# Performance work log

Measured on AMD Instinct MI355X. Metric: run time of the kernel, lower is better.

Reference implementation:

```python
import jax, jax.numpy as jnp
import numpy as np

DYADIC_LEVELS = 3
SIG_LEVEL = 3  # hardcoded depth-3 truncated signature (matches init_kwargs)


def path_signature(inc):
    """Truncated (level-3) path signature of a piecewise-linear path.

    inc: [..., N, d] increments. Returns [..., d + d^2 + d^3] flattened
    signature (levels 1..3, row-major tensor flattening, no scalar term),
    computed via Chen's relation: S <- S (x) exp(dx).
    """
    d = inc.shape[-1]
    bshape = inc.shape[:-2]
    inc_t = jnp.moveaxis(inc, -2, 0)  # [N, ..., d]
    s1 = jnp.zeros(bshape + (d,), inc.dtype)
    s2 = jnp.zeros(bshape + (d, d), inc.dtype)
    s3 = jnp.zeros(bshape + (d, d, d), inc.dtype)

    def step(carry, dx):
        s1, s2, s3 = carry
        dx2 = dx[..., :, None] * dx[..., None, :]          # dx (x) dx
        dx3 = dx2[..., :, :, None] * dx[..., None, None, :]
        n3 = (s3
              + s2[..., :, :, None] * dx[..., None, None, :]
              + 0.5 * s1[..., :, None, None] * dx2[..., None, :, :]
              + dx3 / 6.0)
        n2 = s2 + s1[..., :, None] * dx[..., None, :] + 0.5 * dx2
        n1 = s1 + dx
        return (n1, n2, n3), None

    (s1, s2, s3), _ = jax.lax.scan(step, (s1, s2, s3), inc_t)
    return jnp.concatenate(
        [s1, s2.reshape(bshape + (d * d,)), s3.reshape(bshape + (d * d * d,))],
        axis=-1)


def setup_inputs() -> dict:
    key = jax.random.key(0)
    x = jax.random.normal(key, (64, 1024, 64, 4), dtype=jnp.float32)
    return {"x": x}


def reference(x):
    # x: [batch, frame, element, coords] -> [batch, element, pieces, terms]
    B, T, E, D = x.shape
    xr = jnp.transpose(x, (0, 2, 1, 3))  # [B, E, T, D]
    pieces = []
    for lvl in range(DYADIC_LEVELS + 1):
        P = 2 ** lvl
        L = T // P  # frames per dyadic piece (T divisible by 2**DYADIC_LEVELS)
        xp = xr.reshape(B, E, P, L, D)
        inc = jnp.diff(xp, axis=3)  # [B, E, P, L-1, D]; signatory uses x[start:end]
        pieces.append(path_signature(inc))  # [B, E, P, terms]
    return jnp.concatenate(pieces, axis=2)  # [B, E, 15, 84]
```

## Files before the change

### kernel.cpp

```cpp
#include <hip/hip_runtime.h>

#define DEV __device__ __forceinline__


DEV void sig_step(float s1[4], float s2[16], float s3[64], const float dx[4]) {
    float w[16], u[4], g[4];
#pragma unroll
    for (int j = 0; j < 4; ++j) {
        float hj = 0.5f * dx[j];
        g[j] = s1[j] + hj;
        u[j] = fmaf(dx[j], (1.0f / 3.0f), s1[j]);
#pragma unroll
        for (int k = 0; k < 4; ++k) w[j * 4 + k] = hj * dx[k];
    }
#pragma unroll
    for (int i = 0; i < 4; ++i)
#pragma unroll
        for (int j = 0; j < 4; ++j)
#pragma unroll
            for (int k = 0; k < 4; ++k) {
                float v = s3[i * 16 + j * 4 + k];
                v = fmaf(s2[i * 4 + j], dx[k], v);
                v = fmaf(u[i], w[j * 4 + k], v);
                s3[i * 16 + j * 4 + k] = v;
            }
#pragma unroll
    for (int i = 0; i < 4; ++i)
#pragma unroll
        for (int j = 0; j < 4; ++j)
            s2[i * 4 + j] = fmaf(g[i], dx[j], s2[i * 4 + j]);
#pragma unroll
    for (int i = 0; i < 4; ++i) s1[i] += dx[i];
}

DEV void sig_init(float s1[4], float s2[16], float s3[64], const float dx[4]) {
#pragma unroll
    for (int i = 0; i < 4; ++i) s1[i] = dx[i];
#pragma unroll
    for (int j = 0; j < 4; ++j) {
        float hj = 0.5f * dx[j];
#pragma unroll
        for (int k = 0; k < 4; ++k) s2[j * 4 + k] = hj * dx[k];
    }
#pragma unroll
    for (int i = 0; i < 4; ++i) {
        float ti = dx[i] * (1.0f / 3.0f);
#pragma unroll
        for (int jk = 0; jk < 16; ++jk) s3[i * 16 + jk] = ti * s2[jk];
    }
}

DEV void chen_fold(float a1[4], float a2[16], float a3[64], const float* __restrict__ b) {
    float b1[4], b2[16];
#pragma unroll
    for (int k = 0; k < 4; ++k) b1[k] = b[k * 64];
#pragma unroll
    for (int t = 0; t < 16; ++t) b2[t] = b[(4 + t) * 64];
#pragma unroll
    for (int i = 0; i < 4; ++i)
#pragma unroll
        for (int j = 0; j < 4; ++j)
#pragma unroll
            for (int k = 0; k < 4; ++k) {
                float v = a3[i * 16 + j * 4 + k] + b[(20 + i * 16 + j * 4 + k) * 64];
                v = fmaf(a2[i * 4 + j], b1[k], v);
                v = fmaf(a1[i], b2[j * 4 + k], v);
                a3[i * 16 + j * 4 + k] = v;
            }
#pragma unroll
    for (int i = 0; i < 4; ++i)
#pragma unroll
        for (int j = 0; j < 4; ++j)
            a2[i * 4 + j] = fmaf(a1[i], b1[j], a2[i * 4 + j] + b2[i * 4 + j]);
#pragma unroll
    for (int i = 0; i < 4; ++i) a1[i] += b1[i];
}

DEV void store_sig(float* dst, const float s1[4], const float s2[16], const float s3[64]) {
#pragma unroll
    for (int t = 0; t < 4; ++t) dst[t * 64] = s1[t];
#pragma unroll
    for (int t = 0; t < 16; ++t) dst[(4 + t) * 64] = s2[t];
#pragma unroll
    for (int t = 0; t < 64; ++t) dst[(20 + t) * 64] = s3[t];
}

__global__ __attribute__((amdgpu_flat_work_group_size(256, 256)))
__attribute__((amdgpu_waves_per_eu(2)))
void piece_kernel(const float* __restrict__ x, float* __restrict__ l3sig,
                  float* __restrict__ bdxl3, float* __restrict__ out) {
    __shared__ float sigbuf[2][84][64];
    __shared__ float bdxs[4][4][64];
    const int b = blockIdx.x >> 3;
    const int p = blockIdx.x & 7;
    const int w = threadIdx.x >> 6;
    const int e = threadIdx.x & 63;
    const float4* xf = reinterpret_cast<const float4*>(x);
    const long base = (long)b * 1024 * 64;
    const int c = p * 4 + w;
    const int t0 = c * 32;

    float4 p0 = xf[base + (long)t0 * 64 + e];
    if (c > 0) {
        float4 pm = xf[base + (long)(t0 - 1) * 64 + e];
        float bx[4] = {p0.x - pm.x, p0.y - pm.y, p0.z - pm.z, p0.w - pm.w};
        if (w > 0) {
#pragma unroll
            for (int jj = 0; jj < 4; ++jj) bdxs[w][jj][e] = bx[jj];
        } else {
            float* bb = &bdxl3[(((long)(b * 8 + p)) * 4) * 64 + e];
#pragma unroll
            for (int jj = 0; jj < 4; ++jj) bb[jj * 64] = bx[jj];
        }
    }

    float s1[4], s2[16], s3[64];
    float4 prev = p0;
    float4 cur = xf[base + (long)(t0 + 1) * 64 + e];
    {
        float dx[4] = {cur.x - prev.x, cur.y - prev.y, cur.z - prev.z, cur.w - prev.w};
        sig_init(s1, s2, s3, dx);
        prev = cur;
    }
    float4 nxt = xf[base + (long)(t0 + 2) * 64 + e];
    for (int i = 2; i < 32; ++i) {
        cur = nxt;
        if (i < 31) nxt = xf[base + (long)(t0 + i + 1) * 64 + e];
        float dx[4] = {cur.x - prev.x, cur.y - prev.y, cur.z - prev.z, cur.w - prev.w};
        prev = cur;
        sig_step(s1, s2, s3, dx);
    }

    if (w == 1 || w == 3) store_sig(&sigbuf[w >> 1][0][e], s1, s2, s3);
    __syncthreads();
    if (w == 0 || w == 2) {
        float dxl[4] = {bdxs[w + 1][0][e], bdxs[w + 1][1][e], bdxs[w + 1][2][e], bdxs[w + 1][3][e]};
        sig_step(s1, s2, s3, dxl);
        chen_fold(s1, s2, s3, &sigbuf[w >> 1][0][e]);
    }
    __syncthreads();
    if (w == 2) store_sig(&sigbuf[0][0][e], s1, s2, s3);
    __syncthreads();
    if (w == 0) {
        float dxl[4] = {bdxs[2][0][e], bdxs[2][1][e], bdxs[2][2][e], bdxs[2][3][e]};
        sig_step(s1, s2, s3, dxl);
        chen_fold(s1, s2, s3, &sigbuf[0][0][e]);
        store_sig(&l3sig[(((long)(b * 8 + p)) * 84) * 64 + e], s1, s2, s3);
        float* ob = &out[(((long)(b * 64 + e)) * 15 + 7 + p) * 84];
#pragma unroll
        for (int t = 0; t < 4; ++t) ob[t] = s1[t];
#pragma unroll
        for (int t = 0; t < 16; ++t) ob[4 + t] = s2[t];
#pragma unroll
        for (int t = 0; t < 64; ++t) ob[20 + t] = s3[t];
    }
}

__global__ __attribute__((amdgpu_flat_work_group_size(64, 64)))
__attribute__((amdgpu_waves_per_eu(1)))
void treeB_kernel(const float* __restrict__ l3sig, const float* __restrict__ bdxl3,
                  float* __restrict__ out) {
    const int j = blockIdx.x % 7;
    const int b = blockIdx.x / 7;
    const int e = threadIdx.x;
    int s, n;
    if (j == 0)      { s = 0;           n = 8; }
    else if (j == 1) { s = 0;           n = 4; }
    else if (j == 2) { s = 4;           n = 4; }
    else             { s = (j - 3) * 2; n = 2; }

    float s1[4], s2[16], s3[64];
    {
        const float* src = &l3sig[(((long)(b * 8 + s)) * 84) * 64 + e];
#pragma unroll
        for (int t = 0; t < 4; ++t) s1[t] = src[t * 64];
#pragma unroll
        for (int t = 0; t < 16; ++t) s2[t] = src[(4 + t) * 64];
#pragma unroll
        for (int t = 0; t < 64; ++t) s3[t] = src[(20 + t) * 64];
    }
    for (int q = 1; q < n; ++q) {
        const float* bb = &bdxl3[(((long)(b * 8 + s + q)) * 4) * 64 + e];
        float dx[4] = {bb[0], bb[64], bb[128], bb[192]};
        sig_step(s1, s2, s3, dx);
        chen_fold(s1, s2, s3, &l3sig[(((long)(b * 8 + s + q)) * 84) * 64 + e]);
    }
    float* ob = &out[(((long)(b * 64 + e)) * 15 + j) * 84];
#pragma unroll
    for (int t = 0; t < 4; ++t) ob[t] = s1[t];
#pragma unroll
    for (int t = 0; t < 16; ++t) ob[4 + t] = s2[t];
#pragma unroll
    for (int t = 0; t < 64; ++t) ob[20 + t] = s3[t];
}

__global__ __attribute__((amdgpu_flat_work_group_size(64, 64)))
__attribute__((amdgpu_waves_per_eu(1)))
void direct_kernel(const float* __restrict__ x, float* __restrict__ out) {
    const int pg = blockIdx.x % 15;
    const int b = blockIdx.x / 15;
    const int e = threadIdx.x;
    int lvl, p;
    if (pg == 0)      { lvl = 0; p = 0; }
    else if (pg < 3)  { lvl = 1; p = pg - 1; }
    else if (pg < 7)  { lvl = 2; p = pg - 3; }
    else              { lvl = 3; p = pg - 7; }
    const int L = 1024 >> lvl;
    const int t0 = p * L;
    const float4* xf = reinterpret_cast<const float4*>(x);
    const long base = (long)b * 1024 * 64;

    float4 prev = xf[base + (long)t0 * 64 + e];
    float s1[4], s2[16], s3[64];
    {
        float4 cur = xf[base + (long)(t0 + 1) * 64 + e];
        float dx[4] = {cur.x - prev.x, cur.y - prev.y, cur.z - prev.z, cur.w - prev.w};
        sig_init(s1, s2, s3, dx);
        prev = cur;
    }
    for (int i = 2; i < L; ++i) {
        float4 cur = xf[base + (long)(t0 + i) * 64 + e];
        float dx[4] = {cur.x - prev.x, cur.y - prev.y, cur.z - prev.z, cur.w - prev.w};
        prev = cur;
        sig_step(s1, s2, s3, dx);
    }
    float* ob = &out[(((long)(b * 64 + e)) * 15 + pg) * 84];
#pragma unroll
    for (int t = 0; t < 4; ++t) ob[t] = s1[t];
#pragma unroll
    for (int t = 0; t < 16; ++t) ob[4 + t] = s2[t];
#pragma unroll
    for (int t = 0; t < 64; ++t) ob[20 + t] = s3[t];
}

extern "C" void kernel_launch(void* const* d_in, const int* in_sizes, int n_in,
                              void* d_out, int out_size, void* d_ws, size_t ws_size,
                              hipStream_t stream) {
    (void)in_sizes; (void)n_in; (void)out_size;
    const float* x = (const float*)d_in[0];
    float* out = (float*)d_out;

    const size_t l3_elems = (size_t)64 * 8 * 84 * 64;
    const size_t bdx_elems = (size_t)64 * 8 * 4 * 64;
    const size_t need = (l3_elems + bdx_elems) * sizeof(float);

    if (ws_size >= need) {
        float* l3sig = (float*)d_ws;
        float* bdxl3 = l3sig + l3_elems;
        piece_kernel<<<64 * 8, 256, 0, stream>>>(x, l3sig, bdxl3, out);
        treeB_kernel<<<64 * 7, 64, 0, stream>>>(l3sig, bdxl3, out);
    } else {
        direct_kernel<<<64 * 15, 64, 0, stream>>>(x, out);
    }
}
```

Measured before the change: 43.10 us.

## Restructure tree kernel into shared-memory reduction and deepen input prefetch

The tree kernel previously ran 7 independent blocks per batch, each recomputing Chen folds over up to 8 level-3 pieces. It now runs one 256-thread block per batch that builds the level-2, level-1 and level-0 signatures hierarchically, passing partial results through shared memory. This removes redundant folds and global reads of l3sig. The piece kernel also switches to a 4-deep register ring buffer for input prefetch, with a partially unrolled loop, to hide load latency. The trade-off is fewer blocks (64) in the tree kernel, so less parallelism and more serialization across waves.

```diff
diff --git a/kernel.cpp b/kernel.cpp
--- a/kernel.cpp
+++ b/kernel.cpp
@@ -83,6 +83,24 @@
     for (int t = 0; t < 16; ++t) dst[(4 + t) * 64] = s2[t];
 #pragma unroll
     for (int t = 0; t < 64; ++t) dst[(20 + t) * 64] = s3[t];
+}
+
+DEV void load_sig(const float* src, float s1[4], float s2[16], float s3[64]) {
+#pragma unroll
+    for (int t = 0; t < 4; ++t) s1[t] = src[t * 64];
+#pragma unroll
+    for (int t = 0; t < 16; ++t) s2[t] = src[(4 + t) * 64];
+#pragma unroll
+    for (int t = 0; t < 64; ++t) s3[t] = src[(20 + t) * 64];
+}
+
+DEV void write_out(float* ob, const float s1[4], const float s2[16], const float s3[64]) {
+#pragma unroll
+    for (int t = 0; t < 4; ++t) ob[t] = s1[t];
+#pragma unroll
+    for (int t = 0; t < 16; ++t) ob[4 + t] = s2[t];
+#pragma unroll
+    for (int t = 0; t < 64; ++t) ob[20 + t] = s3[t];
 }
 
 __global__ __attribute__((amdgpu_flat_work_group_size(256, 256)))
@@ -95,15 +113,14 @@
     const int p = blockIdx.x & 7;
     const int w = threadIdx.x >> 6;
     const int e = threadIdx.x & 63;
-    const float4* xf = reinterpret_cast<const float4*>(x);
-    const long base = (long)b * 1024 * 64;
     const int c = p * 4 + w;
-    const int t0 = c * 32;
-
-    float4 p0 = xf[base + (long)t0 * 64 + e];
+    const float4* xp = reinterpret_cast<const float4*>(x)
+                     + (long)b * 65536 + (long)c * 32 * 64 + e;
+
+    float4 prev = xp[0];
     if (c > 0) {
-        float4 pm = xf[base + (long)(t0 - 1) * 64 + e];
-        float bx[4] = {p0.x - pm.x, p0.y - pm.y, p0.z - pm.z, p0.w - pm.w};
+        float4 pm = xp[-64];
+        float bx[4] = {prev.x - pm.x, prev.y - pm.y, prev.z - pm.z, prev.w - pm.w};
         if (w > 0) {
 #pragma unroll
             for (int jj = 0; jj < 4; ++jj) bdxs[w][jj][e] = bx[jj];
@@ -114,18 +131,34 @@
         }
     }
 
+    float4 buf[4];
+#pragma unroll
+    for (int k = 0; k < 4; ++k) buf[k] = xp[(k + 1) * 64];
+
     float s1[4], s2[16], s3[64];
-    float4 prev = p0;
-    float4 cur = xf[base + (long)(t0 + 1) * 64 + e];
     {
+        float4 cur = buf[0];
         float dx[4] = {cur.x - prev.x, cur.y - prev.y, cur.z - prev.z, cur.w - prev.w};
         sig_init(s1, s2, s3, dx);
         prev = cur;
-    }
-    float4 nxt = xf[base + (long)(t0 + 2) * 64 + e];
-    for (int i = 2; i < 32; ++i) {
-        cur = nxt;
-        if (i < 31) nxt = xf[base + (long)(t0 + i + 1) * 64 + e];
+        buf[0] = xp[5 * 64];
+    }
+    for (int ii = 0; ii < 7; ++ii) {
+#pragma unroll
+        for (int j = 0; j < 4; ++j) {
+            const int i = 2 + ii * 4 + j;
+            const int slot = (j + 1) & 3;
+            float4 cur = buf[slot];
+            int li = i + 4; li = li > 31 ? 31 : li;
+            buf[slot] = xp[li * 64];
+            float dx[4] = {cur.x - prev.x, cur.y - prev.y, cur.z - prev.z, cur.w - prev.w};
+            prev = cur;
+            sig_step(s1, s2, s3, dx);
+        }
+    }
+#pragma unroll
+    for (int j = 0; j < 2; ++j) {
+        float4 cur = buf[1 + j];
         float dx[4] = {cur.x - prev.x, cur.y - prev.y, cur.z - prev.z, cur.w - prev.w};
         prev = cur;
         sig_step(s1, s2, s3, dx);
@@ -146,52 +179,49 @@
         sig_step(s1, s2, s3, dxl);
         chen_fold(s1, s2, s3, &sigbuf[0][0][e]);
         store_sig(&l3sig[(((long)(b * 8 + p)) * 84) * 64 + e], s1, s2, s3);
-        float* ob = &out[(((long)(b * 64 + e)) * 15 + 7 + p) * 84];
-#pragma unroll
-        for (int t = 0; t < 4; ++t) ob[t] = s1[t];
-#pragma unroll
-        for (int t = 0; t < 16; ++t) ob[4 + t] = s2[t];
-#pragma unroll
-        for (int t = 0; t < 64; ++t) ob[20 + t] = s3[t];
-    }
-}
-
-__global__ __attribute__((amdgpu_flat_work_group_size(64, 64)))
+        write_out(&out[(((long)(b * 64 + e)) * 15 + 7 + p) * 84], s1, s2, s3);
+    }
+}
+
+__global__ __attribute__((amdgpu_flat_work_group_size(256, 256)))
 __attribute__((amdgpu_waves_per_eu(1)))
 void treeB_kernel(const float* __restrict__ l3sig, const float* __restrict__ bdxl3,
                   float* __restrict__ out) {
-    const int j = blockIdx.x % 7;
-    const int b = blockIdx.x / 7;
-    const int e = threadIdx.x;
-    int s, n;
-    if (j == 0)      { s = 0;           n = 8; }
-    else if (j == 1) { s = 0;           n = 4; }
-    else if (j == 2) { s = 4;           n = 4; }
-    else             { s = (j - 3) * 2; n = 2; }
+    __shared__ float sigbuf[2][84][64];
+    const int b = blockIdx.x;
+    const int w = threadIdx.x >> 6;
+    const int e = threadIdx.x & 63;
 
     float s1[4], s2[16], s3[64];
+    load_sig(&l3sig[(((long)(b * 8 + 2 * w)) * 84) * 64 + e], s1, s2, s3);
     {
-        const float* src = &l3sig[(((long)(b * 8 + s)) * 84) * 64 + e];
-#pragma unroll
-        for (int t = 0; t < 4; ++t) s1[t] = src[t * 64];
-#pragma unroll
-        for (int t = 0; t < 16; ++t) s2[t] = src[(4 + t) * 64];
-#pragma unroll
-        for (int t = 0; t < 64; ++t) s3[t] = src[(20 + t) * 64];
-    }
-    for (int q = 1; q < n; ++q) {
-        const float* bb = &bdxl3[(((long)(b * 8 + s + q)) * 4) * 64 + e];
+        const float* bb = &bdxl3[(((long)(b * 8 + 2 * w + 1)) * 4) * 64 + e];
         float dx[4] = {bb[0], bb[64], bb[128], bb[192]};
         sig_step(s1, s2, s3, dx);
-        chen_fold(s1, s2, s3, &l3sig[(((long)(b * 8 + s + q)) * 84) * 64 + e]);
-    }
-    float* ob = &out[(((long)(b * 64 + e)) * 15 + j) * 84];
-#pragma unroll
-    for (int t = 0; t < 4; ++t) ob[t] = s1[t];
-#pragma unroll
-    for (int t = 0; t < 16; ++t) ob[4 + t] = s2[t];
-#pragma unroll
-    for (int t = 0; t < 64; ++t) ob[20 + t] = s3[t];
+        chen_fold(s1, s2, s3, &l3sig[(((long)(b * 8 + 2 * w + 1)) * 84) * 64 + e]);
+    }
+    write_out(&out[(((long)(b * 64 + e)) * 15 + 3 + w) * 84], s1, s2, s3);
+
+    if (w == 1 || w == 3) store_sig(&sigbuf[w >> 1][0][e], s1, s2, s3);
+    __syncthreads();
+    if (w == 0 || w == 2) {
+        const int jp = (w == 0) ? 2 : 6;
+        const float* bb = &bdxl3[(((long)(b * 8 + jp)) * 4) * 64 + e];
+        float dx[4] = {bb[0], bb[64], bb[128], bb[192]};
+        sig_step(s1, s2, s3, dx);
+        chen_fold(s1, s2, s3, &sigbuf[w >> 1][0][e]);
+        write_out(&out[(((long)(b * 64 + e)) * 15 + 1 + (w >> 1)) * 84], s1, s2, s3);
+    }
+    __syncthreads();
+    if (w == 2) store_sig(&sigbuf[0][0][e], s1, s2, s3);
+    __syncthreads();
+    if (w == 0) {
+        const float* bb = &bdxl3[(((long)(b * 8 + 4)) * 4) * 64 + e];
+        float dx[4] = {bb[0], bb[64], bb[128], bb[192]};
+        sig_step(s1, s2, s3, dx);
+        chen_fold(s1, s2, s3, &sigbuf[0][0][e]);
+        write_out(&out[(((long)(b * 64 + e)) * 15 + 0) * 84], s1, s2, s3);
+    }
 }
 
 __global__ __attribute__((amdgpu_flat_work_group_size(64, 64)))
@@ -208,7 +238,7 @@
     const int L = 1024 >> lvl;
     const int t0 = p * L;
     const float4* xf = reinterpret_cast<const float4*>(x);
-    const long base = (long)b * 1024 * 64;
+    const long base = (long)b * 65536;
 
     float4 prev = xf[base + (long)t0 * 64 + e];
     float s1[4], s2[16], s3[64];
@@ -224,13 +254,7 @@
         prev = cur;
         sig_step(s1, s2, s3, dx);
     }
-    float* ob = &out[(((long)(b * 64 + e)) * 15 + pg) * 84];
-#pragma unroll
-    for (int t = 0; t < 4; ++t) ob[t] = s1[t];
-#pragma unroll
-    for (int t = 0; t < 16; ++t) ob[4 + t] = s2[t];
-#pragma unroll
-    for (int t = 0; t < 64; ++t) ob[20 + t] = s3[t];
+    write_out(&out[(((long)(b * 64 + e)) * 15 + pg) * 84], s1, s2, s3);
 }
 
 extern "C" void kernel_launch(void* const* d_in, const int* in_sizes, int n_in,
@@ -248,7 +272,7 @@
         float* l3sig = (float*)d_ws;
         float* bdxl3 = l3sig + l3_elems;
         piece_kernel<<<64 * 8, 256, 0, stream>>>(x, l3sig, bdxl3, out);
-        treeB_kernel<<<64 * 7, 64, 0, stream>>>(l3sig, bdxl3, out);
+        treeB_kernel<<<64, 256, 0, stream>>>(l3sig, bdxl3, out);
     } else {
         direct_kernel<<<64 * 15, 64, 0, stream>>>(x, out);
     }
```

After: 39.39 us. -8.6%, faster.
